# Performance work log

Hardware: AMD Instinct MI355X
Metric: run time of the kernel (lower is better)

## Reference

```python
import jax, jax.numpy as jnp
import numpy as np

DIM = 512
NUM_HEADS = 8
HEAD_DIM = DIM // NUM_HEADS
SCALE = HEAD_DIM ** -0.5
B, N = 8, 1024


def setup_inputs() -> dict:
    key = jax.random.key(0)
    k1, k2, k3, k4, k5 = jax.random.split(key, 5)
    x = jax.random.normal(k1, (B, N, DIM), dtype=jnp.float32)
    rpe_bias = jax.random.normal(k2, (1, NUM_HEADS, N, N), dtype=jnp.float32)
    # torch Linear weights: [out_features, in_features], y = x @ W.T
    qkv_w = jax.random.normal(k3, (3 * DIM, DIM), dtype=jnp.float32) * (DIM ** -0.5)
    proj_w = jax.random.normal(k4, (DIM, DIM), dtype=jnp.float32) * (DIM ** -0.5)
    proj_b = jax.random.normal(k5, (DIM,), dtype=jnp.float32) * 0.01
    return {"x": x, "rpe_bias": rpe_bias, "qkv_w": qkv_w, "proj_w": proj_w, "proj_b": proj_b}


def reference(x, rpe_bias, qkv_w, proj_w, proj_b):
    b, n, c = x.shape
    h, d = NUM_HEADS, HEAD_DIM
    # qkv projection (no bias): [B,N,3C] -> [3,B,H,N,D]
    qkv = (x @ qkv_w.T).reshape(b, n, 3, h, d).transpose(2, 0, 3, 1, 4)
    q, k, v = qkv[0], qkv[1], qkv[2]
    attn = jnp.einsum('bhnd,bhmd->bhnm', q, k) * SCALE + rpe_bias
    attn = jax.nn.softmax(attn, axis=-1)  # dropout p=0 -> identity
    out = jnp.einsum('bhnm,bhmd->bhnd', attn, v)
    out = out.transpose(0, 2, 1, 3).reshape(b, n, c)
    return out @ proj_w.T + proj_b
```

## Files before the change

### kernel.cpp

```cpp
#include <hip/hip_runtime.h>
#include <hip/hip_bf16.h>

#define B_    8
#define N_    1024
#define DIM_  512
#define H_    8
#define DH_   64
#define SCALE_ 0.125f

typedef unsigned short u16;
typedef __attribute__((ext_vector_type(8))) short bf16x8;
typedef __attribute__((ext_vector_type(4))) float f32x4;
typedef __attribute__((ext_vector_type(4))) _Float16 h16x4;

__device__ __forceinline__ u16 f2bf(float f) {
  union { float f; unsigned u; } v; v.f = f;
  return (u16)((v.u + 0x7fffu + ((v.u >> 16) & 1u)) >> 16);
}
__device__ __forceinline__ unsigned pack2(float a, float b) {
  return (unsigned)f2bf(a) | ((unsigned)f2bf(b) << 16);
}
__device__ __forceinline__ void cp16(const void* g, void* l) {
  __builtin_amdgcn_global_load_lds(
      (const __attribute__((address_space(1))) unsigned*)g,
      (__attribute__((address_space(3))) unsigned*)l, 16, 0, 0);
}

__global__ __launch_bounds__(256) void convert_kernel(
    const float* __restrict__ X, const float* __restrict__ Wq,
    const float* __restrict__ Wp, const float* __restrict__ Bias,
    u16* __restrict__ Xb, u16* __restrict__ Wqb, u16* __restrict__ Wpb,
    _Float16* __restrict__ EB) {
  const int NX4 = (B_ * N_ * DIM_) / 4;
  const int NQ4 = (3 * DIM_ * DIM_) / 4;
  const int NP4 = (DIM_ * DIM_) / 4;
  const int i = blockIdx.x * 256 + threadIdx.x;
  if (i < NX4 + NQ4 + NP4) {
    const float* s; u16* d; int off;
    if (i < NX4)            { s = X;  d = Xb;  off = i; }
    else if (i < NX4 + NQ4) { s = Wq; d = Wqb; off = i - NX4; }
    else                    { s = Wp; d = Wpb; off = i - NX4 - NQ4; }
    float4 f = *(const float4*)(s + (size_t)off * 4);
    uint2 u; u.x = pack2(f.x, f.y); u.y = pack2(f.z, f.w);
    *(uint2*)(d + (size_t)off * 4) = u;
  } else {
    const int off = i - NX4 - NQ4 - NP4;
    float4 f = *(const float4*)(Bias + (size_t)off * 4);
    h16x4 o;
    o[0] = (_Float16)__expf(f.x); o[1] = (_Float16)__expf(f.y);
    o[2] = (_Float16)__expf(f.z); o[3] = (_Float16)__expf(f.w);
    *(h16x4*)(EB + (size_t)off * 4) = o;
  }
}

__global__ __launch_bounds__(256) void qkv_gemm(
    const u16* __restrict__ Ab, const u16* __restrict__ Bb,
    u16* __restrict__ Q, u16* __restrict__ K, u16* __restrict__ Vt) {
  __shared__ __align__(16) u16 smem[128 * 136];
  u16* sA = smem;
  u16* sB = smem + 128 * 64;
  const int t = threadIdx.x;
  const int wv = t >> 6, lane = t & 63, quad = (lane >> 4) & 3, l15 = lane & 15;
  const int wr = wv >> 1, wc = wv & 1;
  const int m0 = blockIdx.y * 128;
  const int n0 = blockIdx.x * 128;

  const int srow = lane >> 3;
  const int schunk = (lane & 7) ^ srow;
  const size_t ga = (size_t)(m0 + srow) * DIM_ + schunk * 8;
  const size_t gb = (size_t)(n0 + srow) * DIM_ + schunk * 8;

  f32x4 zero = {0.f, 0.f, 0.f, 0.f};
  f32x4 acc[4][4];
#pragma unroll
  for (int i = 0; i < 4; i++)
#pragma unroll
    for (int j = 0; j < 4; j++) acc[i][j] = zero;

  for (int k0 = 0; k0 < DIM_; k0 += 64) {
    __syncthreads();
#pragma unroll
    for (int i = 0; i < 4; i++) {
      const int rb = 32 * wv + 8 * i;
      cp16(Ab + ga + (size_t)rb * DIM_ + k0, &sA[rb * 64]);
      cp16(Bb + gb + (size_t)rb * DIM_ + k0, &sB[rb * 64]);
    }
    __syncthreads();
#pragma unroll
    for (int ks = 0; ks < 2; ks++) {
      bf16x8 af[4], bfv[4];
#pragma unroll
      for (int i = 0; i < 4; i++)
        af[i] = *(const bf16x8*)&sA[(wr * 64 + 16 * i + l15) * 64 +
                                    (((ks << 2) | quad) ^ (l15 & 7)) * 8];
#pragma unroll
      for (int j = 0; j < 4; j++)
        bfv[j] = *(const bf16x8*)&sB[(wc * 64 + 16 * j + l15) * 64 +
                                     (((ks << 2) | quad) ^ (l15 & 7)) * 8];
#pragma unroll
      for (int i = 0; i < 4; i++)
#pragma unroll
        for (int j = 0; j < 4; j++)
          acc[i][j] = __builtin_amdgcn_mfma_f32_16x16x32_bf16(af[i], bfv[j], acc[i][j], 0, 0, 0);
    }
  }

  const int tsel = n0 >> 9;
  __syncthreads();
  if (tsel == 2) {
#pragma unroll
    for (int j = 0; j < 4; j++) {
      const int jg = n0 + wc * 64 + 16 * j + l15;
      const int h = (jg >> 6) & 7, d = jg & 63;
#pragma unroll
      for (int i = 0; i < 4; i++) {
        const int mbase = m0 + wr * 64 + 16 * i + quad * 4;
        const int b = mbase >> 10, nb = mbase & 1023;
        ushort4 v4;
        v4.x = f2bf(acc[i][j][0]); v4.y = f2bf(acc[i][j][1]);
        v4.z = f2bf(acc[i][j][2]); v4.w = f2bf(acc[i][j][3]);
        *(ushort4*)&Vt[(((size_t)(b * H_ + h)) * DH_ + d) * N_ + nb] = v4;
      }
    }
  } else {
    const float qs = (tsel == 0) ? SCALE_ : 1.f;
#pragma unroll
    for (int j = 0; j < 4; j++)
#pragma unroll
      for (int i = 0; i < 4; i++)
#pragma unroll
        for (int rr = 0; rr < 4; rr++)
          smem[(wr * 64 + 16 * i + quad * 4 + rr) * 136 + wc * 64 + 16 * j + l15] =
              f2bf(acc[i][j][rr] * qs);
    __syncthreads();
    const int row = t & 127, half = t >> 7;
    const int m = m0 + row;
    const int b = m >> 10, n = m & 1023;
    const int jg0 = n0 + half * 64;
    const int h = (jg0 >> 6) & 7;
    u16* dst = (tsel == 0 ? Q : K) + (((size_t)(b * H_ + h)) * N_ + n) * DH_;
    const u16* srw = &smem[row * 136 + half * 64];
#pragma unroll
    for (int cc = 0; cc < 8; cc++)
      *(uint4*)&dst[cc * 8] = *(const uint4*)&srw[cc * 8];
  }
}

__global__ __launch_bounds__(256) void attn_kernel(
    const u16* __restrict__ Q, const u16* __restrict__ K,
    const u16* __restrict__ Vt, const _Float16* __restrict__ EB,
    u16* __restrict__ AO) {
  __shared__ __align__(16) u16 sQ[64 * 64];
  __shared__ __align__(16) u16 sK[64 * 64];
  __shared__ __align__(16) u16 sV[64 * 64];
  __shared__ __align__(16) u16 sP[64 * 64];
  const int t = threadIdx.x;
  const int wv = t >> 6, lane = t & 63, quad = (lane >> 4) & 3, l15 = lane & 15;
  const int n0 = blockIdx.x << 6;
  const int bh = blockIdx.y, b = bh >> 3, h = bh & 7;
  const int r = t >> 2, cc = t & 3, r7 = r & 7;
  const int slot0 = (((cc << 1)) ^ r7) << 3;
  const int slot1 = (((cc << 1) | 1) ^ r7) << 3;

  const u16* Qb = Q + ((size_t)bh << 10) * DH_;
  const u16* Kb = K + ((size_t)bh << 10) * DH_;
  const u16* Vb = Vt + ((size_t)bh << 6) * N_;

  {
    const u16* src = Qb + (size_t)(n0 + r) * DH_ + cc * 16;
    uint4 a = *(const uint4*)src, b4 = *(const uint4*)(src + 8);
    *(uint4*)&sQ[r * 64 + slot0] = a;
    *(uint4*)&sQ[r * 64 + slot1] = b4;
  }
  uint4 kra = *(const uint4*)(Kb + (size_t)r * DH_ + cc * 16);
  uint4 krb = *(const uint4*)(Kb + (size_t)r * DH_ + cc * 16 + 8);
  uint4 vra = *(const uint4*)(Vb + (size_t)r * N_ + cc * 16);
  uint4 vrb = *(const uint4*)(Vb + (size_t)r * N_ + cc * 16 + 8);

  const int qg = n0 + 16 * wv + l15;
  const _Float16* ebp = EB + ((size_t)h * N_ + qg) * N_ + quad * 4;
  h16x4 ebc[4], ebn[4];
#pragma unroll
  for (int cb = 0; cb < 4; cb++) ebc[cb] = *(const h16x4*)(ebp + 16 * cb);

  f32x4 zero = {0.f, 0.f, 0.f, 0.f};
  f32x4 O[4];
  O[0] = zero; O[1] = zero; O[2] = zero; O[3] = zero;
  float lsum = 0.f;

  for (int kt = 0; kt < 16; kt++) {
    __syncthreads();
    *(uint4*)&sK[r * 64 + slot0] = kra;
    *(uint4*)&sK[r * 64 + slot1] = krb;
    *(uint4*)&sV[r * 64 + slot0] = vra;
    *(uint4*)&sV[r * 64 + slot1] = vrb;
    if (kt < 15) {
      const int m1 = (kt + 1) << 6;
      kra = *(const uint4*)(Kb + (size_t)(m1 + r) * DH_ + cc * 16);
      krb = *(const uint4*)(Kb + (size_t)(m1 + r) * DH_ + cc * 16 + 8);
      vra = *(const uint4*)(Vb + (size_t)r * N_ + m1 + cc * 16);
      vrb = *(const uint4*)(Vb + (size_t)r * N_ + m1 + cc * 16 + 8);
    }
    const int mn = (kt < 15) ? ((kt + 1) << 6) : 0;
#pragma unroll
    for (int cb = 0; cb < 4; cb++) ebn[cb] = *(const h16x4*)(ebp + mn + 16 * cb);
    __syncthreads();

    f32x4 S[4];
    S[0] = zero; S[1] = zero; S[2] = zero; S[3] = zero;
#pragma unroll
    for (int ks = 0; ks < 2; ks++) {
      bf16x8 qf = *(const bf16x8*)&sQ[(16 * wv + l15) * 64 +
                                      ((((ks << 2) | quad) ^ (l15 & 7)) << 3)];
#pragma unroll
      for (int cb = 0; cb < 4; cb++) {
        bf16x8 kf = *(const bf16x8*)&sK[(16 * cb + l15) * 64 +
                                        ((((ks << 2) | quad) ^ (l15 & 7)) << 3)];
        S[cb] = __builtin_amdgcn_mfma_f32_16x16x32_bf16(kf, qf, S[cb], 0, 0, 0);
      }
    }

#pragma unroll
    for (int cb = 0; cb < 4; cb++) {
      const float p0 = __expf(S[cb][0]) * (float)ebc[cb][0];
      const float p1 = __expf(S[cb][1]) * (float)ebc[cb][1];
      const float p2 = __expf(S[cb][2]) * (float)ebc[cb][2];
      const float p3 = __expf(S[cb][3]) * (float)ebc[cb][3];
      lsum += (p0 + p1) + (p2 + p3);
      uint2 pk; pk.x = pack2(p0, p1); pk.y = pack2(p2, p3);
      *(uint2*)&sP[(16 * wv + l15) * 64 +
                   ((((cb << 1) | (quad >> 1)) ^ (l15 & 7)) << 3) + ((quad & 1) << 2)] = pk;
    }
    asm volatile("s_waitcnt lgkmcnt(0)" ::: "memory");

#pragma unroll
    for (int ks = 0; ks < 2; ks++) {
      bf16x8 pf = *(const bf16x8*)&sP[(16 * wv + l15) * 64 +
                                      ((((ks << 2) | quad) ^ (l15 & 7)) << 3)];
#pragma unroll
      for (int db = 0; db < 4; db++) {
        bf16x8 vf = *(const bf16x8*)&sV[(16 * db + l15) * 64 +
                                        ((((ks << 2) | quad) ^ (l15 & 7)) << 3)];
        O[db] = __builtin_amdgcn_mfma_f32_16x16x32_bf16(vf, pf, O[db], 0, 0, 0);
      }
    }
#pragma unroll
    for (int cb = 0; cb < 4; cb++) ebc[cb] = ebn[cb];
  }

  lsum += __shfl_xor(lsum, 16);
  lsum += __shfl_xor(lsum, 32);
  const float inv = 1.f / lsum;
#pragma unroll
  for (int db = 0; db < 4; db++) {
    ushort4 o4;
    o4.x = f2bf(O[db][0] * inv); o4.y = f2bf(O[db][1] * inv);
    o4.z = f2bf(O[db][2] * inv); o4.w = f2bf(O[db][3] * inv);
    *(ushort4*)&AO[(((size_t)b << 10) + qg) * DIM_ + h * DH_ + 16 * db + (quad << 2)] = o4;
  }
}

__global__ __launch_bounds__(256) void proj_gemm(
    const u16* __restrict__ Ab, const u16* __restrict__ Bb,
    const float* __restrict__ Pb, float* __restrict__ Out) {
  __shared__ __align__(16) u16 sA[128 * 64];
  __shared__ __align__(16) u16 sB[128 * 64];
  const int t = threadIdx.x;
  const int wv = t >> 6, lane = t & 63, quad = (lane >> 4) & 3, l15 = lane & 15;
  const int wr = wv >> 1, wc = wv & 1;
  const int m0 = blockIdx.y * 128;
  const int n0 = blockIdx.x * 128;

  const int srow = lane >> 3;
  const int schunk = (lane & 7) ^ srow;
  const size_t ga = (size_t)(m0 + srow) * DIM_ + schunk * 8;
  const size_t gb = (size_t)(n0 + srow) * DIM_ + schunk * 8;

  f32x4 zero = {0.f, 0.f, 0.f, 0.f};
  f32x4 acc[4][4];
#pragma unroll
  for (int i = 0; i < 4; i++)
#pragma unroll
    for (int j = 0; j < 4; j++) acc[i][j] = zero;

  for (int k0 = 0; k0 < DIM_; k0 += 64) {
    __syncthreads();
#pragma unroll
    for (int i = 0; i < 4; i++) {
      const int rb = 32 * wv + 8 * i;
      cp16(Ab + ga + (size_t)rb * DIM_ + k0, &sA[rb * 64]);
      cp16(Bb + gb + (size_t)rb * DIM_ + k0, &sB[rb * 64]);
    }
    __syncthreads();
#pragma unroll
    for (int ks = 0; ks < 2; ks++) {
      bf16x8 af[4], bfv[4];
#pragma unroll
      for (int i = 0; i < 4; i++)
        af[i] = *(const bf16x8*)&sA[(wr * 64 + 16 * i + l15) * 64 +
                                    (((ks << 2) | quad) ^ (l15 & 7)) * 8];
#pragma unroll
      for (int j = 0; j < 4; j++)
        bfv[j] = *(const bf16x8*)&sB[(wc * 64 + 16 * j + l15) * 64 +
                                     (((ks << 2) | quad) ^ (l15 & 7)) * 8];
#pragma unroll
      for (int i = 0; i < 4; i++)
#pragma unroll
        for (int j = 0; j < 4; j++)
          acc[i][j] = __builtin_amdgcn_mfma_f32_16x16x32_bf16(af[i], bfv[j], acc[i][j], 0, 0, 0);
    }
  }

#pragma unroll
  for (int j = 0; j < 4; j++) {
    const int jg = n0 + wc * 64 + 16 * j + l15;
    const float pb = Pb[jg];
#pragma unroll
    for (int i = 0; i < 4; i++) {
      const int mbase = m0 + wr * 64 + 16 * i + quad * 4;
#pragma unroll
      for (int rr = 0; rr < 4; rr++)
        Out[(size_t)(mbase + rr) * DIM_ + jg] = acc[i][j][rr] + pb;
    }
  }
}

extern "C" void kernel_launch(void* const* d_in, const int* in_sizes, int n_in,
                              void* d_out, int out_size, void* d_ws, size_t ws_size,
                              hipStream_t stream) {
  const float* x      = (const float*)d_in[0];
  const float* rpe    = (const float*)d_in[1];
  const float* qkv_w  = (const float*)d_in[2];
  const float* proj_w = (const float*)d_in[3];
  const float* proj_b = (const float*)d_in[4];
  float* out = (float*)d_out;

  const size_t perbuf = (size_t)B_ * N_ * DIM_;
  u16* Xb  = (u16*)d_ws;
  u16* Q   = Xb + perbuf;
  u16* K   = Q + perbuf;
  u16* Vt  = K + perbuf;
  u16* Wqb = Vt + perbuf;
  u16* Wpb = Wqb + (size_t)3 * DIM_ * DIM_;
  _Float16* EB = (_Float16*)(Wpb + (size_t)DIM_ * DIM_);
  u16* AO  = Xb;

  convert_kernel<<<13312, 256, 0, stream>>>(x, qkv_w, proj_w, rpe, Xb, Wqb, Wpb, EB);
  qkv_gemm<<<dim3(12, 64), 256, 0, stream>>>(Xb, Wqb, Q, K, Vt);
  attn_kernel<<<dim3(16, 64), 256, 0, stream>>>(Q, K, Vt, EB, AO);
  proj_gemm<<<dim3(4, 64), 256, 0, stream>>>(AO, Wpb, proj_b, out);
}
```

Measured before the change: 189.4 us.

## Give each attention wave 32 query rows and stage V-transpose stores through LDS

The attention kernel now runs 2 waves per block, each covering 32 query rows as two 16-row groups. Each K and V fragment read from LDS therefore feeds two MFMAs, which cuts LDS traffic per MFMA but needs more registers for the doubled S and O accumulators. Separately, the QKV GEMM's V-transpose epilogue first writes into shared memory and then issues coalesced 16-byte row stores to Vt, replacing scattered 8-byte writes. The extra accumulators add register pressure, and fewer waves per block may reduce latency hiding.

After: 193.8 us. 1.02x slower.

```diff
diff --git a/kernel.cpp b/kernel.cpp
--- a/kernel.cpp
+++ b/kernel.cpp
@@ -109,18 +109,24 @@
   __syncthreads();
   if (tsel == 2) {
 #pragma unroll
-    for (int j = 0; j < 4; j++) {
-      const int jg = n0 + wc * 64 + 16 * j + l15;
-      const int h = (jg >> 6) & 7, d = jg & 63;
+    for (int j = 0; j < 4; j++)
 #pragma unroll
       for (int i = 0; i < 4; i++) {
-        const int mbase = m0 + wr * 64 + 16 * i + quad * 4;
-        const int b = mbase >> 10, nb = mbase & 1023;
         ushort4 v4;
         v4.x = f2bf(acc[i][j][0]); v4.y = f2bf(acc[i][j][1]);
         v4.z = f2bf(acc[i][j][2]); v4.w = f2bf(acc[i][j][3]);
-        *(ushort4*)&Vt[(((size_t)(b * H_ + h)) * DH_ + d) * N_ + nb] = v4;
+        *(ushort4*)&smem[(wc * 64 + 16 * j + l15) * 136 + wr * 64 + 16 * i + quad * 4] = v4;
       }
+    __syncthreads();
+    const int jr = t >> 4, ch = t & 15;
+    const int b = m0 >> 10, nb = (m0 & 1023) + ch * 8;
+#pragma unroll
+    for (int rr = 0; rr < 8; rr++) {
+      const int row = rr * 16 + jr;
+      const int jg = n0 + row;
+      const int h = (jg >> 6) & 7, d = jg & 63;
+      uint4 v = *(const uint4*)&smem[row * 136 + ch * 8];
+      *(uint4*)&Vt[(((size_t)(b * H_ + h)) * DH_ + d) * N_ + nb] = v;
     }
   } else {
     const float qs = (tsel == 0) ? SCALE_ : 1.f;
@@ -146,7 +152,7 @@
   }
 }
 
-__global__ __launch_bounds__(256) void attn_kernel(
+__global__ __launch_bounds__(128) void attn_kernel(
     const u16* __restrict__ Q, const u16* __restrict__ K,
     const u16* __restrict__ Vt, const _Float16* __restrict__ EB,
     u16* __restrict__ AO) {
@@ -158,105 +164,139 @@
   const int wv = t >> 6, lane = t & 63, quad = (lane >> 4) & 3, l15 = lane & 15;
   const int n0 = blockIdx.x << 6;
   const int bh = blockIdx.y, b = bh >> 3, h = bh & 7;
-  const int r = t >> 2, cc = t & 3, r7 = r & 7;
-  const int slot0 = (((cc << 1)) ^ r7) << 3;
-  const int slot1 = (((cc << 1) | 1) ^ r7) << 3;
+  const int r = t >> 1, half = t & 1, r7 = r & 7;
+  const int sl0 = ((((half << 2) | 0) ^ r7) << 3);
+  const int sl1 = ((((half << 2) | 1) ^ r7) << 3);
+  const int sl2 = ((((half << 2) | 2) ^ r7) << 3);
+  const int sl3 = ((((half << 2) | 3) ^ r7) << 3);
 
   const u16* Qb = Q + ((size_t)bh << 10) * DH_;
   const u16* Kb = K + ((size_t)bh << 10) * DH_;
   const u16* Vb = Vt + ((size_t)bh << 6) * N_;
 
   {
-    const u16* src = Qb + (size_t)(n0 + r) * DH_ + cc * 16;
-    uint4 a = *(const uint4*)src, b4 = *(const uint4*)(src + 8);
-    *(uint4*)&sQ[r * 64 + slot0] = a;
-    *(uint4*)&sQ[r * 64 + slot1] = b4;
-  }
-  uint4 kra = *(const uint4*)(Kb + (size_t)r * DH_ + cc * 16);
-  uint4 krb = *(const uint4*)(Kb + (size_t)r * DH_ + cc * 16 + 8);
-  uint4 vra = *(const uint4*)(Vb + (size_t)r * N_ + cc * 16);
-  uint4 vrb = *(const uint4*)(Vb + (size_t)r * N_ + cc * 16 + 8);
-
-  const int qg = n0 + 16 * wv + l15;
-  const _Float16* ebp = EB + ((size_t)h * N_ + qg) * N_ + quad * 4;
-  h16x4 ebc[4], ebn[4];
-#pragma unroll
-  for (int cb = 0; cb < 4; cb++) ebc[cb] = *(const h16x4*)(ebp + 16 * cb);
+    const u16* qs = Qb + (size_t)(n0 + r) * DH_ + half * 32;
+    *(uint4*)&sQ[r * 64 + sl0] = *(const uint4*)(qs + 0);
+    *(uint4*)&sQ[r * 64 + sl1] = *(const uint4*)(qs + 8);
+    *(uint4*)&sQ[r * 64 + sl2] = *(const uint4*)(qs + 16);
+    *(uint4*)&sQ[r * 64 + sl3] = *(const uint4*)(qs + 24);
+  }
+  uint4 kr0, kr1, kr2, kr3, vr0, vr1, vr2, vr3;
+  {
+    const u16* ks = Kb + (size_t)r * DH_ + half * 32;
+    kr0 = *(const uint4*)(ks + 0);  kr1 = *(const uint4*)(ks + 8);
+    kr2 = *(const uint4*)(ks + 16); kr3 = *(const uint4*)(ks + 24);
+    const u16* vs = Vb + (size_t)r * N_ + half * 32;
+    vr0 = *(const uint4*)(vs + 0);  vr1 = *(const uint4*)(vs + 8);
+    vr2 = *(const uint4*)(vs + 16); vr3 = *(const uint4*)(vs + 24);
+  }
+
+  const int qrow = n0 + 32 * wv + l15;
+  const _Float16* ebp0 = EB + ((size_t)h * N_ + qrow) * N_ + (quad << 2);
+  const _Float16* ebp1 = ebp0 + (size_t)16 * N_;
+  h16x4 ebc[2][4], ebn[2][4];
+#pragma unroll
+  for (int cb = 0; cb < 4; cb++) {
+    ebc[0][cb] = *(const h16x4*)(ebp0 + 16 * cb);
+    ebc[1][cb] = *(const h16x4*)(ebp1 + 16 * cb);
+  }
 
   f32x4 zero = {0.f, 0.f, 0.f, 0.f};
-  f32x4 O[4];
-  O[0] = zero; O[1] = zero; O[2] = zero; O[3] = zero;
-  float lsum = 0.f;
+  f32x4 O[2][4];
+#pragma unroll
+  for (int g = 0; g < 2; g++)
+#pragma unroll
+    for (int db = 0; db < 4; db++) O[g][db] = zero;
+  float lsum[2] = {0.f, 0.f};
 
   for (int kt = 0; kt < 16; kt++) {
     __syncthreads();
-    *(uint4*)&sK[r * 64 + slot0] = kra;
-    *(uint4*)&sK[r * 64 + slot1] = krb;
-    *(uint4*)&sV[r * 64 + slot0] = vra;
-    *(uint4*)&sV[r * 64 + slot1] = vrb;
+    *(uint4*)&sK[r * 64 + sl0] = kr0; *(uint4*)&sK[r * 64 + sl1] = kr1;
+    *(uint4*)&sK[r * 64 + sl2] = kr2; *(uint4*)&sK[r * 64 + sl3] = kr3;
+    *(uint4*)&sV[r * 64 + sl0] = vr0; *(uint4*)&sV[r * 64 + sl1] = vr1;
+    *(uint4*)&sV[r * 64 + sl2] = vr2; *(uint4*)&sV[r * 64 + sl3] = vr3;
     if (kt < 15) {
       const int m1 = (kt + 1) << 6;
-      kra = *(const uint4*)(Kb + (size_t)(m1 + r) * DH_ + cc * 16);
-      krb = *(const uint4*)(Kb + (size_t)(m1 + r) * DH_ + cc * 16 + 8);
-      vra = *(const uint4*)(Vb + (size_t)r * N_ + m1 + cc * 16);
-      vrb = *(const uint4*)(Vb + (size_t)r * N_ + m1 + cc * 16 + 8);
+      const u16* ks = Kb + (size_t)(m1 + r) * DH_ + half * 32;
+      kr0 = *(const uint4*)(ks + 0);  kr1 = *(const uint4*)(ks + 8);
+      kr2 = *(const uint4*)(ks + 16); kr3 = *(const uint4*)(ks + 24);
+      const u16* vs = Vb + (size_t)r * N_ + m1 + half * 32;
+      vr0 = *(const uint4*)(vs + 0);  vr1 = *(const uint4*)(vs + 8);
+      vr2 = *(const uint4*)(vs + 16); vr3 = *(const uint4*)(vs + 24);
     }
     const int mn = (kt < 15) ? ((kt + 1) << 6) : 0;
 #pragma unroll
-    for (int cb = 0; cb < 4; cb++) ebn[cb] = *(const h16x4*)(ebp + mn + 16 * cb);
-    __syncthreads();
-
-    f32x4 S[4];
-    S[0] = zero; S[1] = zero; S[2] = zero; S[3] = zero;
+    for (int cb = 0; cb < 4; cb++) {
+      ebn[0][cb] = *(const h16x4*)(ebp0 + mn + 16 * cb);
+      ebn[1][cb] = *(const h16x4*)(ebp1 + mn + 16 * cb);
+    }
+    __syncthreads();
+
+    f32x4 S[2][4];
+#pragma unroll
+    for (int g = 0; g < 2; g++)
+#pragma unroll
+      for (int cb = 0; cb < 4; cb++) S[g][cb] = zero;
 #pragma unroll
     for (int ks = 0; ks < 2; ks++) {
-      bf16x8 qf = *(const bf16x8*)&sQ[(16 * wv + l15) * 64 +
-                                      ((((ks << 2) | quad) ^ (l15 & 7)) << 3)];
+      const int so = ((((ks << 2) | quad) ^ (l15 & 7)) << 3);
+      bf16x8 qf0 = *(const bf16x8*)&sQ[(32 * wv + l15) * 64 + so];
+      bf16x8 qf1 = *(const bf16x8*)&sQ[(32 * wv + 16 + l15) * 64 + so];
 #pragma unroll
       for (int cb = 0; cb < 4; cb++) {
-        bf16x8 kf = *(const bf16x8*)&sK[(16 * cb + l15) * 64 +
-                                        ((((ks << 2) | quad) ^ (l15 & 7)) << 3)];
-        S[cb] = __builtin_amdgcn_mfma_f32_16x16x32_bf16(kf, qf, S[cb], 0, 0, 0);
+        bf16x8 kf = *(const bf16x8*)&sK[(16 * cb + l15) * 64 + so];
+        S[0][cb] = __builtin_amdgcn_mfma_f32_16x16x32_bf16(kf, qf0, S[0][cb], 0, 0, 0);
+        S[1][cb] = __builtin_amdgcn_mfma_f32_16x16x32_bf16(kf, qf1, S[1][cb], 0, 0, 0);
       }
     }
 
 #pragma unroll
-    for (int cb = 0; cb < 4; cb++) {
-      const float p0 = __expf(S[cb][0]) * (float)ebc[cb][0];
-      const float p1 = __expf(S[cb][1]) * (float)ebc[cb][1];
-      const float p2 = __expf(S[cb][2]) * (float)ebc[cb][2];
-      const float p3 = __expf(S[cb][3]) * (float)ebc[cb][3];
-      lsum += (p0 + p1) + (p2 + p3);
-      uint2 pk; pk.x = pack2(p0, p1); pk.y = pack2(p2, p3);
-      *(uint2*)&sP[(16 * wv + l15) * 64 +
-                   ((((cb << 1) | (quad >> 1)) ^ (l15 & 7)) << 3) + ((quad & 1) << 2)] = pk;
-    }
+    for (int g = 0; g < 2; g++)
+#pragma unroll
+      for (int cb = 0; cb < 4; cb++) {
+        const float p0 = __expf(S[g][cb][0]) * (float)ebc[g][cb][0];
+        const float p1 = __expf(S[g][cb][1]) * (float)ebc[g][cb][1];
+        const float p2 = __expf(S[g][cb][2]) * (float)ebc[g][cb][2];
+        const float p3 = __expf(S[g][cb][3]) * (float)ebc[g][cb][3];
+        lsum[g] += (p0 + p1) + (p2 + p3);
+        uint2 pk; pk.x = pack2(p0, p1); pk.y = pack2(p2, p3);
+        *(uint2*)&sP[(32 * wv + 16 * g + l15) * 64 +
+                     ((((cb << 1) | (quad >> 1)) ^ (l15 & 7)) << 3) + ((quad & 1) << 2)] = pk;
+      }
     asm volatile("s_waitcnt lgkmcnt(0)" ::: "memory");
 
 #pragma unroll
     for (int ks = 0; ks < 2; ks++) {
-      bf16x8 pf = *(const bf16x8*)&sP[(16 * wv + l15) * 64 +
-                                      ((((ks << 2) | quad) ^ (l15 & 7)) << 3)];
+      const int so = ((((ks << 2) | quad) ^ (l15 & 7)) << 3);
+      bf16x8 pf0 = *(const bf16x8*)&sP[(32 * wv + l15) * 64 + so];
+      bf16x8 pf1 = *(const bf16x8*)&sP[(32 * wv + 16 + l15) * 64 + so];
 #pragma unroll
       for (int db = 0; db < 4; db++) {
-        bf16x8 vf = *(const bf16x8*)&sV[(16 * db + l15) * 64 +
-                                        ((((ks << 2) | quad) ^ (l15 & 7)) << 3)];
-        O[db] = __builtin_amdgcn_mfma_f32_16x16x32_bf16(vf, pf, O[db], 0, 0, 0);
+        bf16x8 vf = *(const bf16x8*)&sV[(16 * db + l15) * 64 + so];
+        O[0][db] = __builtin_amdgcn_mfma_f32_16x16x32_bf16(vf, pf0, O[0][db], 0, 0, 0);
+        O[1][db] = __builtin_amdgcn_mfma_f32_16x16x32_bf16(vf, pf1, O[1][db], 0, 0, 0);
       }
     }
 #pragma unroll
-    for (int cb = 0; cb < 4; cb++) ebc[cb] = ebn[cb];
-  }
-
-  lsum += __shfl_xor(lsum, 16);
-  lsum += __shfl_xor(lsum, 32);
-  const float inv = 1.f / lsum;
-#pragma unroll
-  for (int db = 0; db < 4; db++) {
-    ushort4 o4;
-    o4.x = f2bf(O[db][0] * inv); o4.y = f2bf(O[db][1] * inv);
-    o4.z = f2bf(O[db][2] * inv); o4.w = f2bf(O[db][3] * inv);
-    *(ushort4*)&AO[(((size_t)b << 10) + qg) * DIM_ + h * DH_ + 16 * db + (quad << 2)] = o4;
+    for (int g = 0; g < 2; g++)
+#pragma unroll
+      for (int cb = 0; cb < 4; cb++) ebc[g][cb] = ebn[g][cb];
+  }
+
+#pragma unroll
+  for (int g = 0; g < 2; g++) {
+    float l = lsum[g];
+    l += __shfl_xor(l, 16);
+    l += __shfl_xor(l, 32);
+    const float inv = 1.f / l;
+    const int qg = n0 + 32 * wv + 16 * g + l15;
+#pragma unroll
+    for (int db = 0; db < 4; db++) {
+      ushort4 o4;
+      o4.x = f2bf(O[g][db][0] * inv); o4.y = f2bf(O[g][db][1] * inv);
+      o4.z = f2bf(O[g][db][2] * inv); o4.w = f2bf(O[g][db][3] * inv);
+      *(ushort4*)&AO[(((size_t)b << 10) + qg) * DIM_ + h * DH_ + 16 * db + (quad << 2)] = o4;
+    }
   }
 }
 
@@ -347,6 +387,6 @@
 
   convert_kernel<<<13312, 256, 0, stream>>>(x, qkv_w, proj_w, rpe, Xb, Wqb, Wpb, EB);
   qkv_gemm<<<dim3(12, 64), 256, 0, stream>>>(Xb, Wqb, Q, K, Vt);
-  attn_kernel<<<dim3(16, 64), 256, 0, stream>>>(Q, K, Vt, EB, AO);
+  attn_kernel<<<dim3(16, 64), 128, 0, stream>>>(Q, K, Vt, EB, AO);
   proj_gemm<<<dim3(4, 64), 256, 0, stream>>>(AO, Wpb, proj_b, out);
 }
```
